# Kernel tuning notes

Measured on AMD Instinct MI355X. Metric: run time of the kernel, lower is better.

## Reference

```python
import jax, jax.numpy as jnp
import numpy as np

N_NODES = 20000
N_EDGES = 320000
X_DIM = 128
EDGE_DIM = 64
HIDDEN = 256
OUT_DIM = 256
LAYERS = 3
N_GRAPHS = 64


def setup_inputs() -> dict:
    key = jax.random.key(0)
    ks = jax.random.split(key, 20)
    x = jax.random.normal(ks[0], (N_NODES, X_DIM), dtype=jnp.float32)
    edge_index = jax.random.randint(ks[1], (2, N_EDGES), 0, N_NODES, dtype=jnp.int64)
    edge_attr = jax.random.normal(ks[2], (N_EDGES, EDGE_DIM), dtype=jnp.float32)
    batch_ids = jnp.sort(jax.random.randint(ks[3], (N_NODES,), 0, N_GRAPHS, dtype=jnp.int64))

    def lin(k, fan_in, fan_out):
        bound = 1.0 / np.sqrt(fan_in)
        kw, kb = jax.random.split(k)
        W = jax.random.uniform(kw, (fan_in, fan_out), minval=-bound, maxval=bound, dtype=jnp.float32)
        b = jax.random.uniform(kb, (fan_out,), minval=-bound, maxval=bound, dtype=jnp.float32)
        return W, b

    xproj_W, xproj_b = lin(ks[4], X_DIM, HIDDEN)
    edge_W, edge_b, mlp_W1, mlp_b1, mlp_W2, mlp_b2 = [], [], [], [], [], []
    for l in range(LAYERS):
        eW, eb = lin(ks[5 + l], EDGE_DIM, HIDDEN)
        w1, b1 = lin(ks[8 + l], HIDDEN, HIDDEN)
        w2, b2 = lin(ks[11 + l], HIDDEN, HIDDEN)
        edge_W.append(eW); edge_b.append(eb)
        mlp_W1.append(w1); mlp_b1.append(b1)
        mlp_W2.append(w2); mlp_b2.append(b2)
    out_W1, out_b1 = lin(ks[14], HIDDEN, HIDDEN)
    out_W2, out_b2 = lin(ks[15], HIDDEN, OUT_DIM)
    return {
        "x": x, "edge_index": edge_index, "edge_attr": edge_attr, "batch_ids": batch_ids,
        "xproj_W": xproj_W, "xproj_b": xproj_b,
        "edge_W": jnp.stack(edge_W), "edge_b": jnp.stack(edge_b),
        "mlp_W1": jnp.stack(mlp_W1), "mlp_b1": jnp.stack(mlp_b1),
        "mlp_W2": jnp.stack(mlp_W2), "mlp_b2": jnp.stack(mlp_b2),
        "out_W1": out_W1, "out_b1": out_b1, "out_W2": out_W2, "out_b2": out_b2,
    }


def reference(x, edge_index, edge_attr, batch_ids, xproj_W, xproj_b,
              edge_W, edge_b, mlp_W1, mlp_b1, mlp_W2, mlp_b2,
              out_W1, out_b1, out_W2, out_b2):
    src, dst = edge_index[0], edge_index[1]
    h = x @ xproj_W + xproj_b  # [N, H]
    for l in range(LAYERS):
        # GINE message: relu(x_j + Lin(edge_attr)), aggregated by sum at target
        msg = jax.nn.relu(h[src] + edge_attr @ edge_W[l] + edge_b[l])  # [E, H]
        agg = jax.ops.segment_sum(msg, dst, num_segments=N_NODES)      # [N, H]
        z = h + agg  # (1 + eps) * x_i with eps = 0
        z = jax.nn.relu(z @ mlp_W1[l] + mlp_b1[l]) @ mlp_W2[l] + mlp_b2[l]
        h = jax.nn.relu(z)  # outer F.relu in forward
    # global mean pool over graphs
    sums = jax.ops.segment_sum(h, batch_ids, num_segments=N_GRAPHS)    # [G, H]
    counts = jax.ops.segment_sum(jnp.ones((h.shape[0],), h.dtype), batch_ids, num_segments=N_GRAPHS)
    g = sums / jnp.maximum(counts, 1.0)[:, None]
    g = jax.nn.relu(g @ out_W1 + out_b1) @ out_W2 + out_b2
    # F.normalize(dim=-1): x / max(||x||_2, eps)
    norm = jnp.maximum(jnp.linalg.norm(g, axis=-1, keepdims=True), 1e-12)
    return g / norm
```

## Files before the change

kernel.cpp:

```cpp
#include <hip/hip_runtime.h>

#define N_NODES 20000
#define N_EDGES 320000
#define X_DIM 128
#define EDGE_DIM 64
#define HIDDEN 256
#define N_GRAPHS 64
#define LAYERS 3

#define NPB 8
#define EB 32
#define ET 4
#define NBLK ((N_NODES + 255) / 256)

typedef __attribute__((ext_vector_type(8))) short short8;
typedef __attribute__((ext_vector_type(4))) float floatx4;

__device__ __forceinline__ unsigned short f2bf(float f) {
    union { float f; unsigned u; } v; v.f = f;
    return (unsigned short)((v.u + 0x7FFFu + ((v.u >> 16) & 1u)) >> 16);
}
__device__ __forceinline__ float bf2f(unsigned short u) {
    return __uint_as_float(((unsigned)u) << 16);
}


__global__ __launch_bounds__(256) void deg_kernel(const int* __restrict__ ei,
                                                  int* __restrict__ deg)
{
    int e = blockIdx.x * 256 + threadIdx.x;
    if (e < N_EDGES) atomicAdd(&deg[ei[N_EDGES + e]], 1);
}

__global__ __launch_bounds__(256) void pscan_kernel(const int* __restrict__ deg,
                                                    int* __restrict__ rp,
                                                    int* __restrict__ bsum)
{
    __shared__ int buf[256];
    const int t = threadIdx.x;
    const int i = blockIdx.x * 256 + t;
    int v = (i < N_NODES) ? deg[i] : 0;
    buf[t] = v;
    __syncthreads();
    for (int off = 1; off < 256; off <<= 1) {
        int a = (t >= off) ? buf[t - off] : 0;
        __syncthreads();
        buf[t] += a;
        __syncthreads();
    }
    if (i < N_NODES) rp[i] = buf[t] - v;
    if (t == 255) bsum[blockIdx.x] = buf[255];
}

__global__ __launch_bounds__(128) void bscan_kernel(const int* __restrict__ bsum,
                                                    int* __restrict__ boff)
{
    __shared__ int buf[128];
    const int t = threadIdx.x;
    int v = (t < NBLK) ? bsum[t] : 0;
    buf[t] = v;
    __syncthreads();
    for (int off = 1; off < 128; off <<= 1) {
        int a = (t >= off) ? buf[t - off] : 0;
        __syncthreads();
        buf[t] += a;
        __syncthreads();
    }
    if (t < NBLK) boff[t] = buf[t] - v;
}

__global__ __launch_bounds__(256) void addoff_kernel(int* __restrict__ rp,
                                                     const int* __restrict__ boff)
{
    const int i = blockIdx.x * 256 + threadIdx.x;
    if (i < N_NODES) rp[i] += boff[blockIdx.x];
    if (i == 0) rp[N_NODES] = N_EDGES;
}

__global__ __launch_bounds__(256) void scatter_kernel(const int* __restrict__ ei,
                                                      const int* __restrict__ rp,
                                                      int* __restrict__ cursor,
                                                      int* __restrict__ perm)
{
    const int e = blockIdx.x * 256 + threadIdx.x;
    if (e < N_EDGES) {
        const int d = ei[N_EDGES + e];
        const int pos = atomicAdd(&cursor[d], 1);
        perm[rp[d] + pos] = e;
    }
}

__global__ __launch_bounds__(256) void permute_kernel(
    const float* __restrict__ ea, const int* __restrict__ ei,
    const int* __restrict__ perm, unsigned short* __restrict__ eab,
    int* __restrict__ srcs, int* __restrict__ dsts)
{
    const int tid = blockIdx.x * 256 + threadIdx.x;
    const int e = tid >> 3, seg = tid & 7;
    const int p = perm[e];
    const float* sp = ea + (size_t)p * EDGE_DIM + seg * 8;
    const float4 v0 = *(const float4*)sp;
    const float4 v1 = *(const float4*)(sp + 4);
    short8 o;
    o[0] = (short)f2bf(v0.x); o[1] = (short)f2bf(v0.y);
    o[2] = (short)f2bf(v0.z); o[3] = (short)f2bf(v0.w);
    o[4] = (short)f2bf(v1.x); o[5] = (short)f2bf(v1.y);
    o[6] = (short)f2bf(v1.z); o[7] = (short)f2bf(v1.w);
    *(short8*)(eab + (size_t)e * EDGE_DIM + seg * 8) = o;
    if (seg == 0) { srcs[e] = ei[p]; dsts[e] = ei[N_EDGES + p]; }
}

__global__ __launch_bounds__(256) void swizzle_kernel(const float* __restrict__ W,
                                                      unsigned short* __restrict__ out,
                                                      int KK)
{
    const int i = blockIdx.x * 256 + threadIdx.x;
    if (i >= 8192 * KK) return;
    const int j = i & 7, lane = (i >> 3) & 63, rem = i >> 9;
    const int kk = rem % KK, rem2 = rem / KK, nt = rem2 & 3, wvv = rem2 >> 2;
    const int n = wvv * 64 + nt * 16 + (lane & 15);
    const int k = kk * 32 + (lane >> 4) * 8 + j;
    out[i] = f2bf(W[k * HIDDEN + n]);
}


__global__ __launch_bounds__(256) void node_proj_kernel(
    const float* __restrict__ x, const float* __restrict__ W,
    const float* __restrict__ b, float* __restrict__ h,
    unsigned short* __restrict__ hbf, float* __restrict__ z)
{
    const int t = threadIdx.x;
    const int row0 = blockIdx.x * NPB;
    __shared__ float xs[NPB][X_DIM];
    for (int idx = t; idx < NPB * X_DIM; idx += 256)
        xs[idx / X_DIM][idx % X_DIM] = x[(size_t)row0 * X_DIM + idx];
    __syncthreads();
    float acc[NPB];
    const float bt = b[t];
#pragma unroll
    for (int r = 0; r < NPB; r++) acc[r] = bt;
    for (int k = 0; k < X_DIM; k++) {
        const float wv = W[k * HIDDEN + t];
#pragma unroll
        for (int r = 0; r < NPB; r++) acc[r] += xs[r][k] * wv;
    }
#pragma unroll
    for (int r = 0; r < NPB; r++) {
        const size_t idx = (size_t)(row0 + r) * HIDDEN + t;
        h[idx] = acc[r];
        hbf[idx] = f2bf(acc[r]);
        z[idx] = 0.f;
    }
}

__global__ __launch_bounds__(256) void edge_mfma_kernel(
    const unsigned short* __restrict__ eab, const int* __restrict__ srcs,
    const int* __restrict__ dsts, const unsigned short* __restrict__ Ws,
    const float* __restrict__ b, const unsigned short* __restrict__ hbf,
    float* __restrict__ z)
{
    const int t = threadIdx.x;
    const int lane = t & 63, wv = t >> 6, q = lane >> 4, m15 = lane & 15;
    __shared__ __align__(16) float msg[EB][260];
    __shared__ int s_src[2][EB], s_dst[2][EB];

    short8 bfr[4][2];
#pragma unroll
    for (int nt = 0; nt < 4; nt++)
#pragma unroll
        for (int kk = 0; kk < 2; kk++)
            bfr[nt][kk] = *(const short8*)(Ws + ((((wv * 4 + nt) * 2 + kk) * 64) + lane) * 8);
    const float bt = b[t];

    if (t < EB) {
        const int e0 = blockIdx.x * ET * EB;
        s_src[0][t] = srcs[e0 + t];
        s_dst[0][t] = dsts[e0 + t];
    }
    __syncthreads();

    for (int tile = 0; tile < ET; tile++) {
        const int cur = tile & 1;
        const int e0 = (blockIdx.x * ET + tile) * EB;

        unsigned short hv[EB];
#pragma unroll
        for (int e = 0; e < EB; e++)
            hv[e] = hbf[(size_t)s_src[cur][e] * HIDDEN + t];

        if (tile + 1 < ET && t < EB) {
            s_src[1 - cur][t] = srcs[e0 + EB + t];
            s_dst[1 - cur][t] = dsts[e0 + EB + t];
        }

        floatx4 acc[2][4];
#pragma unroll
        for (int mt = 0; mt < 2; mt++)
#pragma unroll
            for (int nt = 0; nt < 4; nt++)
                acc[mt][nt] = (floatx4){0.f, 0.f, 0.f, 0.f};
#pragma unroll
        for (int kk = 0; kk < 2; kk++) {
            const short8 a0 = *(const short8*)(eab + (size_t)(e0 + m15) * EDGE_DIM + kk * 32 + q * 8);
            const short8 a1 = *(const short8*)(eab + (size_t)(e0 + 16 + m15) * EDGE_DIM + kk * 32 + q * 8);
#pragma unroll
            for (int nt = 0; nt < 4; nt++) {
                acc[0][nt] = __builtin_amdgcn_mfma_f32_16x16x32_bf16(a0, bfr[nt][kk], acc[0][nt], 0, 0, 0);
                acc[1][nt] = __builtin_amdgcn_mfma_f32_16x16x32_bf16(a1, bfr[nt][kk], acc[1][nt], 0, 0, 0);
            }
        }
#pragma unroll
        for (int mt = 0; mt < 2; mt++)
#pragma unroll
            for (int nt = 0; nt < 4; nt++)
#pragma unroll
                for (int r = 0; r < 4; r++)
                    msg[mt * 16 + q * 4 + r][wv * 64 + nt * 16 + m15] = acc[mt][nt][r];
        __syncthreads();

        float s = 0.f;
        int prev = s_dst[cur][0];
#pragma unroll
        for (int e = 0; e < EB; e++) {
            const int d = s_dst[cur][e];
            if (d != prev) {
                atomicAdd(&z[(size_t)prev * HIDDEN + t], s);
                s = 0.f; prev = d;
            }
            const float m = msg[e][t] + bt + bf2f(hv[e]);
            s += m > 0.f ? m : 0.f;
        }
        atomicAdd(&z[(size_t)prev * HIDDEN + t], s);
        __syncthreads();
    }
}

__global__ __launch_bounds__(256) void mlp_mfma_kernel(
    const unsigned short* __restrict__ W1s, const float* __restrict__ b1,
    const unsigned short* __restrict__ W2s, const float* __restrict__ b2,
    float* __restrict__ h, float* __restrict__ z, unsigned short* __restrict__ hbf)
{
    const int t = threadIdx.x;
    const int lane = t & 63, wv = t >> 6, q = lane >> 4, m15 = lane & 15;
    const int row0 = blockIdx.x * 32;
    __shared__ __align__(16) unsigned short zs[32][264];

#pragma unroll
    for (int r = 0; r < 32; r++) {
        const size_t idx = (size_t)(row0 + r) * HIDDEN + t;
        zs[r][t] = f2bf(h[idx] + z[idx]);
        z[idx] = 0.f;
    }
    __syncthreads();

    float b1v[4], b2v[4];
#pragma unroll
    for (int nt = 0; nt < 4; nt++) {
        const int c = wv * 64 + nt * 16 + m15;
        b1v[nt] = b1[c]; b2v[nt] = b2[c];
    }

    floatx4 acc[2][4];
#pragma unroll
    for (int mt = 0; mt < 2; mt++)
#pragma unroll
        for (int nt = 0; nt < 4; nt++)
            acc[mt][nt] = (floatx4){0.f, 0.f, 0.f, 0.f};

#pragma unroll
    for (int kk = 0; kk < 8; kk++) {
        short8 bfr[4];
#pragma unroll
        for (int nt = 0; nt < 4; nt++)
            bfr[nt] = *(const short8*)(W1s + ((((wv * 4 + nt) * 8 + kk) * 64) + lane) * 8);
        const short8 a0 = *(const short8*)&zs[m15][kk * 32 + q * 8];
        const short8 a1 = *(const short8*)&zs[16 + m15][kk * 32 + q * 8];
#pragma unroll
        for (int nt = 0; nt < 4; nt++) {
            acc[0][nt] = __builtin_amdgcn_mfma_f32_16x16x32_bf16(a0, bfr[nt], acc[0][nt], 0, 0, 0);
            acc[1][nt] = __builtin_amdgcn_mfma_f32_16x16x32_bf16(a1, bfr[nt], acc[1][nt], 0, 0, 0);
        }
    }
    __syncthreads();
#pragma unroll
    for (int mt = 0; mt < 2; mt++)
#pragma unroll
        for (int nt = 0; nt < 4; nt++)
#pragma unroll
            for (int r = 0; r < 4; r++) {
                const int row = mt * 16 + q * 4 + r, c = wv * 64 + nt * 16 + m15;
                const float v = acc[mt][nt][r] + b1v[nt];
                zs[row][c] = f2bf(v > 0.f ? v : 0.f);
            }
    __syncthreads();

#pragma unroll
    for (int mt = 0; mt < 2; mt++)
#pragma unroll
        for (int nt = 0; nt < 4; nt++)
            acc[mt][nt] = (floatx4){0.f, 0.f, 0.f, 0.f};

#pragma unroll
    for (int kk = 0; kk < 8; kk++) {
        short8 bfr[4];
#pragma unroll
        for (int nt = 0; nt < 4; nt++)
            bfr[nt] = *(const short8*)(W2s + ((((wv * 4 + nt) * 8 + kk) * 64) + lane) * 8);
        const short8 a0 = *(const short8*)&zs[m15][kk * 32 + q * 8];
        const short8 a1 = *(const short8*)&zs[16 + m15][kk * 32 + q * 8];
#pragma unroll
        for (int nt = 0; nt < 4; nt++) {
            acc[0][nt] = __builtin_amdgcn_mfma_f32_16x16x32_bf16(a0, bfr[nt], acc[0][nt], 0, 0, 0);
            acc[1][nt] = __builtin_amdgcn_mfma_f32_16x16x32_bf16(a1, bfr[nt], acc[1][nt], 0, 0, 0);
        }
    }
#pragma unroll
    for (int mt = 0; mt < 2; mt++)
#pragma unroll
        for (int nt = 0; nt < 4; nt++)
#pragma unroll
            for (int r = 0; r < 4; r++) {
                const int row = mt * 16 + q * 4 + r, c = wv * 64 + nt * 16 + m15;
                float v = acc[mt][nt][r] + b2v[nt];
                v = v > 0.f ? v : 0.f;
                const size_t idx = (size_t)(row0 + row) * HIDDEN + c;
                h[idx] = v;
                hbf[idx] = f2bf(v);
            }
}

__global__ __launch_bounds__(256) void pool_kernel(
    const float* __restrict__ h, const int* __restrict__ bid,
    float* __restrict__ gout)
{
    const int g = blockIdx.x;
    const int t = threadIdx.x;
    int lo = 0, hi = N_NODES;
    while (lo < hi) { int mid = (lo + hi) >> 1; if (bid[mid] < g) lo = mid + 1; else hi = mid; }
    const int start = lo;
    hi = N_NODES;
    while (lo < hi) { int mid = (lo + hi) >> 1; if (bid[mid] < g + 1) lo = mid + 1; else hi = mid; }
    const int end = lo;
    float s = 0.f;
    for (int i = start; i < end; i++) s += h[(size_t)i * HIDDEN + t];
    const float cnt = (float)(end - start);
    gout[g * HIDDEN + t] = s / (cnt > 1.f ? cnt : 1.f);
}

__global__ __launch_bounds__(256) void head_kernel(
    const float* __restrict__ gin, const float* __restrict__ W1,
    const float* __restrict__ b1, const float* __restrict__ W2,
    const float* __restrict__ b2, float* __restrict__ out)
{
    const int g = blockIdx.x;
    const int t = threadIdx.x;
    __shared__ float gs[HIDDEN];
    __shared__ float t1[HIDDEN];
    __shared__ float red[256];
    gs[t] = gin[g * HIDDEN + t];
    __syncthreads();
    float acc = b1[t];
    for (int k = 0; k < HIDDEN; k++) acc += gs[k] * W1[k * HIDDEN + t];
    t1[t] = acc > 0.f ? acc : 0.f;
    __syncthreads();
    float acc2 = b2[t];
    for (int k = 0; k < HIDDEN; k++) acc2 += t1[k] * W2[k * HIDDEN + t];
    red[t] = acc2 * acc2;
    __syncthreads();
    for (int s = 128; s > 0; s >>= 1) {
        if (t < s) red[t] += red[t + s];
        __syncthreads();
    }
    float norm = sqrtf(red[0]);
    norm = norm > 1e-12f ? norm : 1e-12f;
    out[g * HIDDEN + t] = acc2 / norm;
}

extern "C" void kernel_launch(void* const* d_in, const int* in_sizes, int n_in,
                              void* d_out, int out_size, void* d_ws, size_t ws_size,
                              hipStream_t stream)
{
    const float* x   = (const float*)d_in[0];
    const int*   ei  = (const int*)d_in[1];
    const float* ea  = (const float*)d_in[2];
    const int*   bid = (const int*)d_in[3];
    const float* xW  = (const float*)d_in[4];
    const float* xb  = (const float*)d_in[5];
    const float* eW  = (const float*)d_in[6];
    const float* eb  = (const float*)d_in[7];
    const float* W1  = (const float*)d_in[8];
    const float* b1  = (const float*)d_in[9];
    const float* W2  = (const float*)d_in[10];
    const float* b2  = (const float*)d_in[11];
    const float* oW1 = (const float*)d_in[12];
    const float* ob1 = (const float*)d_in[13];
    const float* oW2 = (const float*)d_in[14];
    const float* ob2 = (const float*)d_in[15];
    float* out = (float*)d_out;

    char* p = (char*)d_ws;
    auto alloc = [&](size_t bytes) { char* r = p; p += (bytes + 255) & ~(size_t)255; return r; };
    float* h     = (float*)alloc((size_t)N_NODES * HIDDEN * 4);
    float* z     = (float*)alloc((size_t)N_NODES * HIDDEN * 4);
    float* gpool = (float*)alloc((size_t)N_GRAPHS * HIDDEN * 4);
    int* deg     = (int*)alloc(N_NODES * 4);
    int* rowptr  = (int*)alloc((N_NODES + 1) * 4);
    int* cursor  = (int*)alloc(N_NODES * 4);
    int* bsum    = (int*)alloc(NBLK * 4);
    int* boff    = (int*)alloc(NBLK * 4);
    int* perm    = (int*)alloc((size_t)N_EDGES * 4);
    int* srcs    = (int*)alloc((size_t)N_EDGES * 4);
    int* dsts    = (int*)alloc((size_t)N_EDGES * 4);
    unsigned short* hbf = (unsigned short*)alloc((size_t)N_NODES * HIDDEN * 2);
    unsigned short* eab = (unsigned short*)alloc((size_t)N_EDGES * EDGE_DIM * 2);
    unsigned short* eWs = (unsigned short*)alloc((size_t)LAYERS * EDGE_DIM * HIDDEN * 2);
    unsigned short* W1s = (unsigned short*)alloc((size_t)LAYERS * HIDDEN * HIDDEN * 2);
    unsigned short* W2s = (unsigned short*)alloc((size_t)LAYERS * HIDDEN * HIDDEN * 2);

    hipMemsetAsync(deg, 0, N_NODES * sizeof(int), stream);
    hipMemsetAsync(cursor, 0, N_NODES * sizeof(int), stream);
    deg_kernel<<<(N_EDGES + 255) / 256, 256, 0, stream>>>(ei, deg);
    pscan_kernel<<<NBLK, 256, 0, stream>>>(deg, rowptr, bsum);
    bscan_kernel<<<1, 128, 0, stream>>>(bsum, boff);
    addoff_kernel<<<NBLK, 256, 0, stream>>>(rowptr, boff);
    scatter_kernel<<<(N_EDGES + 255) / 256, 256, 0, stream>>>(ei, rowptr, cursor, perm);
    permute_kernel<<<(N_EDGES * 8) / 256, 256, 0, stream>>>(ea, ei, perm, eab, srcs, dsts);
    for (int l = 0; l < LAYERS; l++) {
        swizzle_kernel<<<64, 256, 0, stream>>>(eW + (size_t)l * EDGE_DIM * HIDDEN,
                                               eWs + (size_t)l * EDGE_DIM * HIDDEN, 2);
        swizzle_kernel<<<256, 256, 0, stream>>>(W1 + (size_t)l * HIDDEN * HIDDEN,
                                                W1s + (size_t)l * HIDDEN * HIDDEN, 8);
        swizzle_kernel<<<256, 256, 0, stream>>>(W2 + (size_t)l * HIDDEN * HIDDEN,
                                                W2s + (size_t)l * HIDDEN * HIDDEN, 8);
    }

    node_proj_kernel<<<N_NODES / NPB, 256, 0, stream>>>(x, xW, xb, h, hbf, z);
    for (int l = 0; l < LAYERS; l++) {
        edge_mfma_kernel<<<N_EDGES / (EB * ET), 256, 0, stream>>>(
            eab, srcs, dsts, eWs + (size_t)l * EDGE_DIM * HIDDEN,
            eb + l * HIDDEN, hbf, z);
        mlp_mfma_kernel<<<N_NODES / 32, 256, 0, stream>>>(
            W1s + (size_t)l * HIDDEN * HIDDEN, b1 + l * HIDDEN,
            W2s + (size_t)l * HIDDEN * HIDDEN, b2 + l * HIDDEN, h, z, hbf);
    }
    pool_kernel<<<N_GRAPHS, 256, 0, stream>>>(h, bid, gpool);
    head_kernel<<<N_GRAPHS, 256, 0, stream>>>(gpool, oW1, ob1, oW2, ob2, out);
}
```

Baseline: 659.0 us.

## Shrink edge message tile to bf16, carry segment sums across tiles, split pooling

The edge kernel now stores the per-tile message matrix in shared memory as bf16 rather than fp32, halving LDS use, and requests higher occupancy via launch bounds. The running destination sum is carried across the four edge tiles, so atomics fire only at destination changes instead of once per tile. Global mean pooling is split into eight chunks per graph combined by atomic adds, with the division by count moved into the head kernel. The bf16 message storage adds rounding error, and the launch-bounds hint may force register spills.

New measurement: 1.254 ms. +90.3%, slower.

```diff
diff --git a/kernel.cpp b/kernel.cpp
--- a/kernel.cpp
+++ b/kernel.cpp
@@ -11,6 +11,7 @@
 #define NPB 8
 #define EB 32
 #define ET 4
+#define PSPLIT 8
 #define NBLK ((N_NODES + 255) / 256)
 
 typedef __attribute__((ext_vector_type(8))) short short8;
@@ -153,7 +154,7 @@
     }
 }
 
-__global__ __launch_bounds__(256) void edge_mfma_kernel(
+__global__ __launch_bounds__(256, 8) void edge_mfma_kernel(
     const unsigned short* __restrict__ eab, const int* __restrict__ srcs,
     const int* __restrict__ dsts, const unsigned short* __restrict__ Ws,
     const float* __restrict__ b, const unsigned short* __restrict__ hbf,
@@ -161,7 +162,7 @@
 {
     const int t = threadIdx.x;
     const int lane = t & 63, wv = t >> 6, q = lane >> 4, m15 = lane & 15;
-    __shared__ __align__(16) float msg[EB][260];
+    __shared__ unsigned short msg[EB][264];
     __shared__ int s_src[2][EB], s_dst[2][EB];
 
     short8 bfr[4][2];
@@ -178,6 +179,9 @@
         s_dst[0][t] = dsts[e0 + t];
     }
     __syncthreads();
+
+    float s = 0.f;
+    int prev = s_dst[0][0];
 
     for (int tile = 0; tile < ET; tile++) {
         const int cur = tile & 1;
@@ -215,11 +219,9 @@
             for (int nt = 0; nt < 4; nt++)
 #pragma unroll
                 for (int r = 0; r < 4; r++)
-                    msg[mt * 16 + q * 4 + r][wv * 64 + nt * 16 + m15] = acc[mt][nt][r];
-        __syncthreads();
-
-        float s = 0.f;
-        int prev = s_dst[cur][0];
+                    msg[mt * 16 + q * 4 + r][wv * 64 + nt * 16 + m15] = f2bf(acc[mt][nt][r]);
+        __syncthreads();
+
 #pragma unroll
         for (int e = 0; e < EB; e++) {
             const int d = s_dst[cur][e];
@@ -227,12 +229,12 @@
                 atomicAdd(&z[(size_t)prev * HIDDEN + t], s);
                 s = 0.f; prev = d;
             }
-            const float m = msg[e][t] + bt + bf2f(hv[e]);
+            const float m = bf2f(msg[e][t]) + bt + bf2f(hv[e]);
             s += m > 0.f ? m : 0.f;
         }
-        atomicAdd(&z[(size_t)prev * HIDDEN + t], s);
-        __syncthreads();
-    }
+        __syncthreads();
+    }
+    atomicAdd(&z[(size_t)prev * HIDDEN + t], s);
 }
 
 __global__ __launch_bounds__(256) void mlp_mfma_kernel(
@@ -331,9 +333,10 @@
 
 __global__ __launch_bounds__(256) void pool_kernel(
     const float* __restrict__ h, const int* __restrict__ bid,
-    float* __restrict__ gout)
-{
-    const int g = blockIdx.x;
+    float* __restrict__ gsum)
+{
+    const int g = blockIdx.x / PSPLIT;
+    const int part = blockIdx.x % PSPLIT;
     const int t = threadIdx.x;
     int lo = 0, hi = N_NODES;
     while (lo < hi) { int mid = (lo + hi) >> 1; if (bid[mid] < g) lo = mid + 1; else hi = mid; }
@@ -341,23 +344,35 @@
     hi = N_NODES;
     while (lo < hi) { int mid = (lo + hi) >> 1; if (bid[mid] < g + 1) lo = mid + 1; else hi = mid; }
     const int end = lo;
+    const int len = end - start;
+    const int chunk = (len + PSPLIT - 1) / PSPLIT;
+    const int s0 = start + part * chunk;
+    const int s1 = min(s0 + chunk, end);
+    if (s0 >= s1) return;
     float s = 0.f;
-    for (int i = start; i < end; i++) s += h[(size_t)i * HIDDEN + t];
-    const float cnt = (float)(end - start);
-    gout[g * HIDDEN + t] = s / (cnt > 1.f ? cnt : 1.f);
+    for (int i = s0; i < s1; i++) s += h[(size_t)i * HIDDEN + t];
+    atomicAdd(&gsum[g * HIDDEN + t], s);
 }
 
 __global__ __launch_bounds__(256) void head_kernel(
-    const float* __restrict__ gin, const float* __restrict__ W1,
-    const float* __restrict__ b1, const float* __restrict__ W2,
-    const float* __restrict__ b2, float* __restrict__ out)
+    const float* __restrict__ gsum, const int* __restrict__ bid,
+    const float* __restrict__ W1, const float* __restrict__ b1,
+    const float* __restrict__ W2, const float* __restrict__ b2,
+    float* __restrict__ out)
 {
     const int g = blockIdx.x;
     const int t = threadIdx.x;
     __shared__ float gs[HIDDEN];
     __shared__ float t1[HIDDEN];
     __shared__ float red[256];
-    gs[t] = gin[g * HIDDEN + t];
+    int lo = 0, hi = N_NODES;
+    while (lo < hi) { int mid = (lo + hi) >> 1; if (bid[mid] < g) lo = mid + 1; else hi = mid; }
+    const int start = lo;
+    hi = N_NODES;
+    while (lo < hi) { int mid = (lo + hi) >> 1; if (bid[mid] < g + 1) lo = mid + 1; else hi = mid; }
+    float cnt = (float)(lo - start);
+    cnt = cnt > 1.f ? cnt : 1.f;
+    gs[t] = gsum[g * HIDDEN + t] / cnt;
     __syncthreads();
     float acc = b1[t];
     for (int k = 0; k < HIDDEN; k++) acc += gs[k] * W1[k * HIDDEN + t];
@@ -419,6 +434,7 @@
 
     hipMemsetAsync(deg, 0, N_NODES * sizeof(int), stream);
     hipMemsetAsync(cursor, 0, N_NODES * sizeof(int), stream);
+    hipMemsetAsync(gpool, 0, N_GRAPHS * HIDDEN * sizeof(float), stream);
     deg_kernel<<<(N_EDGES + 255) / 256, 256, 0, stream>>>(ei, deg);
     pscan_kernel<<<NBLK, 256, 0, stream>>>(deg, rowptr, bsum);
     bscan_kernel<<<1, 128, 0, stream>>>(bsum, boff);
@@ -443,6 +459,6 @@
             W1s + (size_t)l * HIDDEN * HIDDEN, b1 + l * HIDDEN,
             W2s + (size_t)l * HIDDEN * HIDDEN, b2 + l * HIDDEN, h, z, hbf);
     }
-    pool_kernel<<<N_GRAPHS, 256, 0, stream>>>(h, bid, gpool);
-    head_kernel<<<N_GRAPHS, 256, 0, stream>>>(gpool, oW1, ob1, oW2, ob2, out);
-}
+    pool_kernel<<<N_GRAPHS * PSPLIT, 256, 0, stream>>>(h, bid, gpool);
+    head_kernel<<<N_GRAPHS, 256, 0, stream>>>(gpool, bid, oW1, ob1, oW2, ob2, out);
+}
```
